# Optimization experiments

Hardware: AMD Instinct MI355X
Metric: run time of the kernel (lower is better)

Reference implementation:

```python
import jax, jax.numpy as jnp
import numpy as np

H = 768
NH = 12
HD = 64
R = 4
SCALING = 8.0 / 4.0  # lora_alpha / r


def setup_inputs() -> dict:
    key = jax.random.key(0)
    ks = jax.random.split(key, 16)
    B, T = 16, 512
    s = 0.02
    x = jax.random.normal(ks[0], (B, T, H), dtype=jnp.float32)
    mask = jax.random.randint(ks[1], (B, T), 0, 2, dtype=jnp.int32)
    return {
        "x": x,
        "mask": mask,
        "Wq": jax.random.normal(ks[2], (H, H), jnp.float32) * s,
        "bq": jnp.zeros((H,), jnp.float32),
        "Aq": jax.random.normal(ks[3], (R, H), jnp.float32) * s,
        "Bq": jax.random.normal(ks[4], (H, R), jnp.float32) * s,
        "Wk": jax.random.normal(ks[5], (H, H), jnp.float32) * s,
        "bk": jnp.zeros((H,), jnp.float32),
        "Wv": jax.random.normal(ks[6], (H, H), jnp.float32) * s,
        "bv": jnp.zeros((H,), jnp.float32),
        "Av": jax.random.normal(ks[7], (R, H), jnp.float32) * s,
        "Bv": jax.random.normal(ks[8], (H, R), jnp.float32) * s,
        "Wo": jax.random.normal(ks[9], (H, H), jnp.float32) * s,
        "bo": jnp.zeros((H,), jnp.float32),
    }


def _lora_linear(x, W, b, A, Bm):
    # base: x @ W^T + b ; lora: (x @ A^T) @ B^T * scaling (dropout inactive at eval)
    return x @ W.T + b + (x @ A.T) @ Bm.T * SCALING


def reference(x, mask, Wq, bq, Aq, Bq, Wk, bk, Wv, bv, Av, Bv, Wo, bo):
    B, T, _ = x.shape
    q = _lora_linear(x, Wq, bq, Aq, Bq).reshape(B, T, NH, HD).transpose(0, 2, 1, 3)
    k = (x @ Wk.T + bk).reshape(B, T, NH, HD).transpose(0, 2, 1, 3)
    v = _lora_linear(x, Wv, bv, Av, Bv).reshape(B, T, NH, HD).transpose(0, 2, 1, 3)
    # [B, NH, T, T]
    scores = jnp.einsum("bhqd,bhkd->bhqk", q, k) / jnp.sqrt(jnp.float32(HD))
    m = (mask == 0)[:, None, None, :]  # mask key positions where mask==0
    scores = jnp.where(m, jnp.float32(-1e9), scores)
    attn = jax.nn.softmax(scores, axis=-1)  # dropout inactive at eval
    out = jnp.einsum("bhqk,bhkd->bhqd", attn, v)
    out = out.transpose(0, 2, 1, 3).reshape(B, T, H)
    return out @ Wo.T + bo
```

## Files before the change

kernel.cpp:

```cpp
#include <hip/hip_runtime.h>
#include <stdint.h>

#define H 768
#define NHEAD 12
#define HDIM 64
#define BATCH 16
#define TSEQ 512
#define BT (BATCH*TSEQ)
#define C3 (3*H)
#define LDQK 1536

typedef __attribute__((ext_vector_type(8))) short short8;
typedef __attribute__((ext_vector_type(4))) float floatx4;
typedef unsigned short u16;

__device__ __forceinline__ u16 f2bf(float f) {
    union { float f; unsigned int u; } v; v.f = f;
    unsigned int u = v.u;
    return (u16)((u + 0x7FFFu + ((u >> 16) & 1u)) >> 16);
}

__device__ __forceinline__ void async_ld16(const void* g, void* l) {
    __builtin_amdgcn_global_load_lds((__attribute__((address_space(1))) void*)g,
                                     (__attribute__((address_space(3))) void*)l,
                                     16, 0, 0);
}

__global__ void prep_weights(const float* __restrict__ Wq, const float* __restrict__ bq,
                             const float* __restrict__ Aq, const float* __restrict__ Bq,
                             const float* __restrict__ Wk, const float* __restrict__ bk,
                             const float* __restrict__ Wv, const float* __restrict__ bv,
                             const float* __restrict__ Av, const float* __restrict__ Bv,
                             const float* __restrict__ Wo,
                             u16* __restrict__ Wall, u16* __restrict__ Wobf,
                             float* __restrict__ bias_all)
{
    const int idx = blockIdx.x * 256 + threadIdx.x;
    const int r = idx / H;
    const int c = idx - r * H;
    if (r < H) {
        float v = Wq[idx] + 2.0f * (Bq[r*4+0]*Aq[c] + Bq[r*4+1]*Aq[H+c] +
                                    Bq[r*4+2]*Aq[2*H+c] + Bq[r*4+3]*Aq[3*H+c]);
        Wall[idx] = f2bf(v);
    } else if (r < 2*H) {
        Wall[idx] = f2bf(Wk[idx - H*H]);
    } else if (r < 3*H) {
        const int rr = r - 2*H;
        float v = Wv[rr*H + c] + 2.0f * (Bv[rr*4+0]*Av[c] + Bv[rr*4+1]*Av[H+c] +
                                         Bv[rr*4+2]*Av[2*H+c] + Bv[rr*4+3]*Av[3*H+c]);
        Wall[idx] = f2bf(v);
    } else {
        Wobf[idx - 3*H*H] = f2bf(Wo[idx - 3*H*H]);
    }
    if (idx < C3) {
        bias_all[idx] = (idx < H) ? bq[idx] : (idx < 2*H ? bk[idx - H] : bv[idx - 2*H]);
    }
}

__global__ void cvt_x_kernel(const float* __restrict__ x, u16* __restrict__ xb)
{
    const int i = (blockIdx.x * 256 + threadIdx.x) * 4;
    const float4 v = *(const float4*)(x + i);
    u16 o[4] = { f2bf(v.x), f2bf(v.y), f2bf(v.z), f2bf(v.w) };
    *(uint2*)(xb + i) = *(const uint2*)o;
}

template<int MODE>
__global__ __launch_bounds__(256)
void gemm_bt(const u16* __restrict__ A, const u16* __restrict__ Bw,
             const float* __restrict__ bias, void* __restrict__ Cout,
             u16* __restrict__ Vout, int K, int ldc)
{
    __shared__ u16 Ablk[128 * 64];
    __shared__ u16 Bblk[128 * 64];
    const int tid  = threadIdx.x;
    const int wave = tid >> 6;
    const int lane = tid & 63;
    const int quad = lane >> 4;
    const int l16  = lane & 15;
    const int m0 = blockIdx.y * 128;
    const int n0 = blockIdx.x * 128;
    const int mw = (wave & 1) * 64;
    const int nw = (wave >> 1) * 64;

    const int r8 = lane >> 3;
    const int kgs = ((lane & 7) ^ r8) * 8;
    const u16* gA = A  + (size_t)(m0 + wave*32 + r8) * K + kgs;
    const u16* gB = Bw + (size_t)(n0 + wave*32 + r8) * K + kgs;
    u16* lA = Ablk + wave * 32 * 64;
    u16* lB = Bblk + wave * 32 * 64;

    floatx4 acc[4][4] = {};
    const int sw = l16 & 7;

    for (int k0 = 0; k0 < K; k0 += 64) {
        __syncthreads();
        #pragma unroll
        for (int j = 0; j < 4; j++) {
            async_ld16(gA + k0 + (size_t)(j*8) * K, lA + j*8*64);
            async_ld16(gB + k0 + (size_t)(j*8) * K, lB + j*8*64);
        }
        __syncthreads();
        #pragma unroll
        for (int kk = 0; kk < 2; kk++) {
            short8 af[4], bfr[4];
            #pragma unroll
            for (int mt = 0; mt < 4; mt++)
                af[mt] = *(const short8*)(Ablk + (mw + mt*16 + l16)*64 + ((quad + 4*kk) ^ sw)*8);
            #pragma unroll
            for (int nt = 0; nt < 4; nt++)
                bfr[nt] = *(const short8*)(Bblk + (nw + nt*16 + l16)*64 + ((quad + 4*kk) ^ sw)*8);
            #pragma unroll
            for (int mt = 0; mt < 4; mt++)
                #pragma unroll
                for (int nt = 0; nt < 4; nt++)
                    acc[mt][nt] = __builtin_amdgcn_mfma_f32_16x16x32_bf16(af[mt], bfr[nt], acc[mt][nt], 0, 0, 0);
        }
    }

    if (MODE == 1 && n0 >= LDQK) {
        const int nv = n0 + nw - LDQK + 0;
        const int b  = m0 >> 9;
        #pragma unroll
        for (int nt = 0; nt < 4; nt++) {
            const int n  = nv + nt*16 + l16;
            const int hh = n >> 6, d = n & 63;
            const float bv = bias[LDQK + n];
            u16* vp = Vout + ((size_t)(b*NHEAD + hh) * HDIM + d) * TSEQ;
            #pragma unroll
            for (int mt = 0; mt < 4; mt++) {
                const int t0 = (m0 & 511) + mw + mt*16 + quad*4;
                u16 pack[4];
                #pragma unroll
                for (int r = 0; r < 4; r++) pack[r] = f2bf(acc[mt][nt][r] + bv);
                *(uint2*)(vp + t0) = *(const uint2*)pack;
            }
        }
    } else {
        #pragma unroll
        for (int nt = 0; nt < 4; nt++) {
            const int n = n0 + nw + nt*16 + l16;
            const float bv = bias[n];
            #pragma unroll
            for (int mt = 0; mt < 4; mt++) {
                #pragma unroll
                for (int r = 0; r < 4; r++) {
                    const int m = m0 + mw + mt*16 + quad*4 + r;
                    const float v = acc[mt][nt][r] + bv;
                    if (MODE == 1) ((u16*)Cout)[(size_t)m * ldc + n] = f2bf(v);
                    else           ((float*)Cout)[(size_t)m * ldc + n] = v;
                }
            }
        }
    }
}

#define PSTRIDE 40

__global__ __launch_bounds__(256, 3)
void attn_kernel(const u16* __restrict__ qk, const u16* __restrict__ vt,
                 const int* __restrict__ mask, u16* __restrict__ attn_out)
{
    __shared__ float maskadd[TSEQ];
    __shared__ u16 Pbuf[4][2][16 * PSTRIDE];

    const int qt = blockIdx.x;
    const int bh = blockIdx.y;
    const int b = bh / NHEAD, h = bh - b * NHEAD;
    const int tid  = threadIdx.x;
    const int wave = tid >> 6;
    const int lane = tid & 63;
    const int quad = lane >> 4;
    const int l16  = lane & 15;

    for (int i = tid; i < TSEQ; i += 256)
        maskadd[i] = (mask[b*TSEQ + i] == 0) ? -1e9f : 0.0f;
    __syncthreads();

    const size_t btok = (size_t)b * TSEQ;
    const int q0 = qt * 128 + wave * 32;

    short8 qf[2][2];
    #pragma unroll
    for (int m = 0; m < 2; m++) {
        const u16* qp = qk + (btok + q0 + m*16 + l16) * LDQK + h*HDIM + quad*8;
        qf[m][0] = *(const short8*)qp;
        qf[m][1] = *(const short8*)(qp + 32);
    }

    const u16* kbase = qk + btok * LDQK + H + h*HDIM + quad*8;
    const u16* vbase = vt + (size_t)bh * HDIM * TSEQ + quad*8;

    floatx4 o[2][4] = {};
    float lsum[2][4] = {};

    auto loadKV = [&](int kb, short8* kf, short8* vf) {
        const u16* kp0 = kbase + (size_t)(kb + l16) * LDQK;
        const u16* kp1 = kbase + (size_t)(kb + 16 + l16) * LDQK;
        kf[0] = *(const short8*)kp0;
        kf[1] = *(const short8*)(kp0 + 32);
        kf[2] = *(const short8*)kp1;
        kf[3] = *(const short8*)(kp1 + 32);
        #pragma unroll
        for (int d = 0; d < 4; d++)
            vf[d] = *(const short8*)(vbase + (size_t)(d*16 + l16) * TSEQ + kb);
    };

    auto compute = [&](int kb, const short8* kf, const short8* vf) {
        floatx4 s[2][2];
        #pragma unroll
        for (int m = 0; m < 2; m++)
            #pragma unroll
            for (int t = 0; t < 2; t++) {
                floatx4 acc = {0.f, 0.f, 0.f, 0.f};
                acc = __builtin_amdgcn_mfma_f32_16x16x32_bf16(qf[m][0], kf[t*2+0], acc, 0, 0, 0);
                acc = __builtin_amdgcn_mfma_f32_16x16x32_bf16(qf[m][1], kf[t*2+1], acc, 0, 0, 0);
                s[m][t] = acc;
            }
        const float m0 = maskadd[kb + l16];
        const float m1 = maskadd[kb + 16 + l16];
        #pragma unroll
        for (int m = 0; m < 2; m++) {
            u16* Pw = Pbuf[wave][m];
            #pragma unroll
            for (int r = 0; r < 4; r++) {
                const float p0 = __expf(s[m][0][r] * 0.125f + m0);
                const float p1 = __expf(s[m][1][r] * 0.125f + m1);
                lsum[m][r] += p0 + p1;
                Pw[(quad*4 + r) * PSTRIDE + l16]      = f2bf(p0);
                Pw[(quad*4 + r) * PSTRIDE + 16 + l16] = f2bf(p1);
            }
        }
        #pragma unroll
        for (int m = 0; m < 2; m++) {
            const short8 pa = *(const short8*)(Pbuf[wave][m] + l16 * PSTRIDE + quad*8);
            #pragma unroll
            for (int d = 0; d < 4; d++)
                o[m][d] = __builtin_amdgcn_mfma_f32_16x16x32_bf16(pa, vf[d], o[m][d], 0, 0, 0);
        }
    };

    short8 kA[4], vA[4], kB[4], vB[4];
    loadKV(0, kA, vA);
    for (int kb = 0; kb < TSEQ - 64; kb += 64) {
        loadKV(kb + 32, kB, vB);
        compute(kb, kA, vA);
        loadKV(kb + 64, kA, vA);
        compute(kb + 32, kB, vB);
    }
    loadKV(TSEQ - 32, kB, vB);
    compute(TSEQ - 64, kA, vA);
    compute(TSEQ - 32, kB, vB);

    #pragma unroll
    for (int m = 0; m < 2; m++) {
        float inv[4];
        #pragma unroll
        for (int r = 0; r < 4; r++) {
            float l = lsum[m][r];
            l += __shfl_xor(l, 1);
            l += __shfl_xor(l, 2);
            l += __shfl_xor(l, 4);
            l += __shfl_xor(l, 8);
            inv[r] = 1.0f / l;
        }
        #pragma unroll
        for (int d = 0; d < 4; d++)
            #pragma unroll
            for (int r = 0; r < 4; r++) {
                const int q = q0 + m*16 + quad*4 + r;
                attn_out[(btok + q) * H + h*HDIM + d*16 + l16] = f2bf(o[m][d][r] * inv[r]);
            }
    }
}

extern "C" void kernel_launch(void* const* d_in, const int* in_sizes, int n_in,
                              void* d_out, int out_size, void* d_ws, size_t ws_size,
                              hipStream_t stream)
{
    const float* x   = (const float*)d_in[0];
    const int* mask  = (const int*)d_in[1];
    const float* Wq  = (const float*)d_in[2];
    const float* bq  = (const float*)d_in[3];
    const float* Aq  = (const float*)d_in[4];
    const float* Bq  = (const float*)d_in[5];
    const float* Wk  = (const float*)d_in[6];
    const float* bk  = (const float*)d_in[7];
    const float* Wv  = (const float*)d_in[8];
    const float* bv  = (const float*)d_in[9];
    const float* Av  = (const float*)d_in[10];
    const float* Bv  = (const float*)d_in[11];
    const float* Wo  = (const float*)d_in[12];
    const float* bo  = (const float*)d_in[13];

    char* ws = (char*)d_ws;
    u16*   xb      = (u16*)  (ws);
    u16*   Wall    = (u16*)  (ws + 12582912);
    u16*   Wobf    = (u16*)  (ws + 16121856);
    float* biasall = (float*)(ws + 17301504);
    u16*   qk      = (u16*)  (ws + 17310720);
    u16*   vt      = (u16*)  (ws + 42476544);
    u16*   attn_o  = (u16*)  (ws + 55059456);

    prep_weights<<<(4*H*H)/256, 256, 0, stream>>>(Wq, bq, Aq, Bq, Wk, bk, Wv, bv,
                                                  Av, Bv, Wo, Wall, Wobf, biasall);
    cvt_x_kernel<<<(BT*H)/1024, 256, 0, stream>>>(x, xb);
    gemm_bt<1><<<dim3(C3/128, BT/128), 256, 0, stream>>>(xb, Wall, biasall, qk, vt, H, LDQK);
    attn_kernel<<<dim3(TSEQ/128, BATCH*NHEAD), 256, 0, stream>>>(qk, vt, mask, attn_o);
    gemm_bt<0><<<dim3(H/128, BT/128), 256, 0, stream>>>(attn_o, Wobf, bo, d_out, nullptr, H, H);
}
```

Before: 228.5 us.

## Stage attention K/V through double-buffered LDS and shrink GEMM K-tile to 32

Measured after the change: 223.9 us. 1.02x faster.

```diff
diff --git a/kernel.cpp b/kernel.cpp
--- a/kernel.cpp
+++ b/kernel.cpp
@@ -71,8 +71,8 @@
              const float* __restrict__ bias, void* __restrict__ Cout,
              u16* __restrict__ Vout, int K, int ldc)
 {
-    __shared__ u16 Ablk[128 * 64];
-    __shared__ u16 Bblk[128 * 64];
+    __shared__ u16 Ablk[128 * 32];
+    __shared__ u16 Bblk[128 * 32];
     const int tid  = threadIdx.x;
     const int wave = tid >> 6;
     const int lane = tid & 63;
@@ -83,43 +83,39 @@
     const int mw = (wave & 1) * 64;
     const int nw = (wave >> 1) * 64;
 
-    const int r8 = lane >> 3;
-    const int kgs = ((lane & 7) ^ r8) * 8;
-    const u16* gA = A  + (size_t)(m0 + wave*32 + r8) * K + kgs;
-    const u16* gB = Bw + (size_t)(n0 + wave*32 + r8) * K + kgs;
-    u16* lA = Ablk + wave * 32 * 64;
-    u16* lB = Bblk + wave * 32 * 64;
+    const int srow = lane >> 2;
+    const int scol = ((lane & 3) ^ ((lane >> 3) & 3)) * 8;
+    const u16* gA = A  + (size_t)(m0 + wave*32 + srow) * K + scol;
+    const u16* gB = Bw + (size_t)(n0 + wave*32 + srow) * K + scol;
+    u16* lA = Ablk + wave * 32 * 32;
+    u16* lB = Bblk + wave * 32 * 32;
 
     floatx4 acc[4][4] = {};
-    const int sw = l16 & 7;
-
-    for (int k0 = 0; k0 < K; k0 += 64) {
+    const int rsw = ((l16 >> 1) & 3);
+
+    for (int k0 = 0; k0 < K; k0 += 32) {
         __syncthreads();
-        #pragma unroll
-        for (int j = 0; j < 4; j++) {
-            async_ld16(gA + k0 + (size_t)(j*8) * K, lA + j*8*64);
-            async_ld16(gB + k0 + (size_t)(j*8) * K, lB + j*8*64);
-        }
+        async_ld16(gA + k0,          lA);
+        async_ld16(gA + k0 + 16*K,   lA + 16*32);
+        async_ld16(gB + k0,          lB);
+        async_ld16(gB + k0 + 16*K,   lB + 16*32);
         __syncthreads();
-        #pragma unroll
-        for (int kk = 0; kk < 2; kk++) {
-            short8 af[4], bfr[4];
-            #pragma unroll
-            for (int mt = 0; mt < 4; mt++)
-                af[mt] = *(const short8*)(Ablk + (mw + mt*16 + l16)*64 + ((quad + 4*kk) ^ sw)*8);
+        short8 af[4], bfr[4];
+        #pragma unroll
+        for (int mt = 0; mt < 4; mt++)
+            af[mt] = *(const short8*)(Ablk + (mw + mt*16 + l16)*32 + ((quad ^ rsw)*8));
+        #pragma unroll
+        for (int nt = 0; nt < 4; nt++)
+            bfr[nt] = *(const short8*)(Bblk + (nw + nt*16 + l16)*32 + ((quad ^ rsw)*8));
+        #pragma unroll
+        for (int mt = 0; mt < 4; mt++)
             #pragma unroll
             for (int nt = 0; nt < 4; nt++)
-                bfr[nt] = *(const short8*)(Bblk + (nw + nt*16 + l16)*64 + ((quad + 4*kk) ^ sw)*8);
-            #pragma unroll
-            for (int mt = 0; mt < 4; mt++)
-                #pragma unroll
-                for (int nt = 0; nt < 4; nt++)
-                    acc[mt][nt] = __builtin_amdgcn_mfma_f32_16x16x32_bf16(af[mt], bfr[nt], acc[mt][nt], 0, 0, 0);
-        }
+                acc[mt][nt] = __builtin_amdgcn_mfma_f32_16x16x32_bf16(af[mt], bfr[nt], acc[mt][nt], 0, 0, 0);
     }
 
     if (MODE == 1 && n0 >= LDQK) {
-        const int nv = n0 + nw - LDQK + 0;
+        const int nv = n0 + nw - LDQK;
         const int b  = m0 >> 9;
         #pragma unroll
         for (int nt = 0; nt < 4; nt++) {
@@ -157,11 +153,13 @@
 
 #define PSTRIDE 40
 
-__global__ __launch_bounds__(256, 3)
+__global__ __launch_bounds__(256)
 void attn_kernel(const u16* __restrict__ qk, const u16* __restrict__ vt,
                  const int* __restrict__ mask, u16* __restrict__ attn_out)
 {
     __shared__ float maskadd[TSEQ];
+    __shared__ u16 Kbuf[2][32 * 64];
+    __shared__ u16 Vbuf[2][64 * 32];
     __shared__ u16 Pbuf[4][2][16 * PSTRIDE];
 
     const int qt = blockIdx.x;
@@ -175,7 +173,6 @@
 
     for (int i = tid; i < TSEQ; i += 256)
         maskadd[i] = (mask[b*TSEQ + i] == 0) ? -1e9f : 0.0f;
-    __syncthreads();
 
     const size_t btok = (size_t)b * TSEQ;
     const int q0 = qt * 128 + wave * 32;
@@ -188,33 +185,49 @@
         qf[m][1] = *(const short8*)(qp + 32);
     }
 
-    const u16* kbase = qk + btok * LDQK + H + h*HDIM + quad*8;
-    const u16* vbase = vt + (size_t)bh * HDIM * TSEQ + quad*8;
+    const u16* kglob = qk + btok * LDQK + H + h*HDIM;
+    const u16* vglob = vt + (size_t)bh * HDIM * TSEQ;
+
+    auto stage = [&](int kb, int pp) {
+        {
+            const int r = lane >> 3;
+            const int g = (lane & 7) ^ r;
+            async_ld16(kglob + (size_t)(kb + wave*8 + r) * LDQK + g*8,
+                       &Kbuf[pp][wave*8*64]);
+        }
+        {
+            const int dr = lane >> 2;
+            const int g  = (lane & 3) ^ ((dr >> 1) & 3);
+            async_ld16(vglob + (size_t)(wave*16 + dr) * TSEQ + kb + g*8,
+                       &Vbuf[pp][wave*16*32]);
+        }
+    };
 
     floatx4 o[2][4] = {};
     float lsum[2][4] = {};
 
-    auto loadKV = [&](int kb, short8* kf, short8* vf) {
-        const u16* kp0 = kbase + (size_t)(kb + l16) * LDQK;
-        const u16* kp1 = kbase + (size_t)(kb + 16 + l16) * LDQK;
-        kf[0] = *(const short8*)kp0;
-        kf[1] = *(const short8*)(kp0 + 32);
-        kf[2] = *(const short8*)kp1;
-        kf[3] = *(const short8*)(kp1 + 32);
-        #pragma unroll
-        for (int d = 0; d < 4; d++)
-            vf[d] = *(const short8*)(vbase + (size_t)(d*16 + l16) * TSEQ + kb);
-    };
-
-    auto compute = [&](int kb, const short8* kf, const short8* vf) {
+    auto compute = [&](int kb, int pp) {
+        const u16* Kb_ = Kbuf[pp];
+        const u16* Vb_ = Vbuf[pp];
+        short8 kf[2][2];
+        #pragma unroll
+        for (int t = 0; t < 2; t++)
+            #pragma unroll
+            for (int h2 = 0; h2 < 2; h2++)
+                kf[t][h2] = *(const short8*)(Kb_ + (t*16 + l16)*64 + (((h2*4 + quad) ^ (l16 & 7))*8));
+        short8 vf[4];
+        #pragma unroll
+        for (int dt = 0; dt < 4; dt++)
+            vf[dt] = *(const short8*)(Vb_ + (dt*16 + l16)*32 + ((quad ^ ((l16 >> 1) & 3))*8));
+
         floatx4 s[2][2];
         #pragma unroll
         for (int m = 0; m < 2; m++)
             #pragma unroll
             for (int t = 0; t < 2; t++) {
                 floatx4 acc = {0.f, 0.f, 0.f, 0.f};
-                acc = __builtin_amdgcn_mfma_f32_16x16x32_bf16(qf[m][0], kf[t*2+0], acc, 0, 0, 0);
-                acc = __builtin_amdgcn_mfma_f32_16x16x32_bf16(qf[m][1], kf[t*2+1], acc, 0, 0, 0);
+                acc = __builtin_amdgcn_mfma_f32_16x16x32_bf16(qf[m][0], kf[t][0], acc, 0, 0, 0);
+                acc = __builtin_amdgcn_mfma_f32_16x16x32_bf16(qf[m][1], kf[t][1], acc, 0, 0, 0);
                 s[m][t] = acc;
             }
         const float m0 = maskadd[kb + l16];
@@ -235,22 +248,17 @@
         for (int m = 0; m < 2; m++) {
             const short8 pa = *(const short8*)(Pbuf[wave][m] + l16 * PSTRIDE + quad*8);
             #pragma unroll
-            for (int d = 0; d < 4; d++)
-                o[m][d] = __builtin_amdgcn_mfma_f32_16x16x32_bf16(pa, vf[d], o[m][d], 0, 0, 0);
+            for (int dt = 0; dt < 4; dt++)
+                o[m][dt] = __builtin_amdgcn_mfma_f32_16x16x32_bf16(pa, vf[dt], o[m][dt], 0, 0, 0);
         }
     };
 
-    short8 kA[4], vA[4], kB[4], vB[4];
-    loadKV(0, kA, vA);
-    for (int kb = 0; kb < TSEQ - 64; kb += 64) {
-        loadKV(kb + 32, kB, vB);
-        compute(kb, kA, vA);
-        loadKV(kb + 64, kA, vA);
-        compute(kb + 32, kB, vB);
-    }
-    loadKV(TSEQ - 32, kB, vB);
-    compute(TSEQ - 64, kA, vA);
-    compute(TSEQ - 32, kB, vB);
+    stage(0, 0);
+    for (int it = 0; it < 16; it++) {
+        __syncthreads();
+        if (it < 15) stage((it + 1) * 32, (it + 1) & 1);
+        compute(it * 32, it & 1);
+    }
 
     #pragma unroll
     for (int m = 0; m < 2; m++) {
@@ -265,11 +273,11 @@
             inv[r] = 1.0f / l;
         }
         #pragma unroll
-        for (int d = 0; d < 4; d++)
+        for (int dt = 0; dt < 4; dt++)
             #pragma unroll
             for (int r = 0; r < 4; r++) {
                 const int q = q0 + m*16 + quad*4 + r;
-                attn_out[(btok + q) * H + h*HDIM + d*16 + l16] = f2bf(o[m][d][r] * inv[r]);
+                attn_out[(btok + q) * H + h*HDIM + dt*16 + l16] = f2bf(o[m][dt][r] * inv[r]);
             }
     }
 }
```
